# Kernel optimization log

Hardware: AMD Instinct MI355X
Metric: run time of the kernel (lower is better)

Reference implementation:

```python
import jax, jax.numpy as jnp
import numpy as np
import math

B, T, C, H = 2, 2048, 1024, 16
HD = C // H

def setup_inputs() -> dict:
    key = jax.random.key(0)
    ks = jax.random.split(key, 5)
    s_in = 1.0 / math.sqrt(C)
    x = jax.random.normal(ks[0], (B, T, C), dtype=jnp.float32)
    W_attn = jax.random.normal(ks[1], (C, 3 * C), dtype=jnp.float32) * s_in
    b_attn = jnp.zeros((3 * C,), dtype=jnp.float32)
    W_proj = jax.random.normal(ks[2], (C, C), dtype=jnp.float32) * s_in
    b_proj = jnp.zeros((C,), dtype=jnp.float32)
    return {"x": x, "W_attn": W_attn, "b_attn": b_attn, "W_proj": W_proj, "b_proj": b_proj}

def reference(x, W_attn, b_attn, W_proj, b_proj):
    Bx, Tx, Cx = x.shape
    c = x @ W_attn + b_attn  # [B,T,3C]
    q, k, v = jnp.split(c, 3, axis=2)
    # [B,T,H,hd] -> [B,H,T,hd]
    q = q.reshape(Bx, Tx, H, HD).transpose(0, 2, 1, 3)
    k = k.reshape(Bx, Tx, H, HD).transpose(0, 2, 1, 3)
    v = v.reshape(Bx, Tx, H, HD).transpose(0, 2, 1, 3)
    # NOTE: module scales by 1/sqrt(C), not 1/sqrt(head_dim)
    attn = jnp.einsum('bhqd,bhkd->bhqk', q, k) * (1.0 / math.sqrt(Cx))
    causal = jnp.tril(jnp.ones((Tx, Tx), dtype=bool))
    attn = jnp.where(causal[None, None], attn, -jnp.inf)
    attn = jax.nn.softmax(attn, axis=-1)
    y = jnp.einsum('bhqk,bhkd->bhqd', attn, v)
    y = y.transpose(0, 2, 1, 3).reshape(Bx, Tx, Cx)
    return y @ W_proj + b_proj
```

## Files before the change

### kernel.cpp

```cpp
#include <hip/hip_runtime.h>
#include <math.h>

#define Bv 2
#define Tv 2048
#define Cv 1024
#define Hv 16
#define HDv 64
#define Mv (Bv * Tv)
#define SZv (Bv * Hv * Tv * HDv)

typedef short bf16x8 __attribute__((ext_vector_type(8)));
typedef float f32x4 __attribute__((ext_vector_type(4)));

static __device__ __forceinline__ unsigned short f2bf(float f) {
    unsigned u = __float_as_uint(f);
    u += 0x7fffu + ((u >> 16) & 1u);
    return (unsigned short)(u >> 16);
}

static __device__ __forceinline__ unsigned f2bf2(float a, float b) {
    unsigned r;
    asm("v_cvt_pk_bf16_f32 %0, %1, %2" : "=v"(r) : "v"(a), "v"(b));
    return r;
}

#define AS1 __attribute__((address_space(1)))
#define AS3 __attribute__((address_space(3)))
#define GLD16(gp, lp) __builtin_amdgcn_global_load_lds( \
    (AS1 const void*)(const void*)(gp), (AS3 void*)(void*)(lp), 16, 0, 0)

#define WAITVM(n) asm volatile("s_waitcnt vmcnt(" #n ")" ::: "memory")
#define WAITLGKM0 asm volatile("s_waitcnt lgkmcnt(0)" ::: "memory")
#define BARRIER   asm volatile("s_barrier" ::: "memory")

__global__ __launch_bounds__(256) void prep_kernel(
    const float* __restrict__ x, const float* __restrict__ Wa,
    const float* __restrict__ Wp,
    unsigned short* __restrict__ xB, unsigned short* __restrict__ WaT,
    unsigned short* __restrict__ WpT)
{
    __shared__ float tile[32][33];
    const int bid = blockIdx.x;
    const int tid = threadIdx.x;

    if (bid < 4096) {
        int i = bid * 256 + tid;
        float4 f = ((const float4*)x)[i];
        ushort4 u;
        u.x = f2bf(f.x); u.y = f2bf(f.y); u.z = f2bf(f.z); u.w = f2bf(f.w);
        ((ushort4*)xB)[i] = u;
        return;
    }
    const float* src; unsigned short* dst; int Ncols, bi;
    if (bid < 7168) { bi = bid - 4096; Ncols = 3072; src = Wa; dst = WaT; }
    else            { bi = bid - 7168; Ncols = 1024; src = Wp; dst = WpT; }
    const int nct = Ncols / 32;
    const int c0 = (bi % nct) * 32, r0 = (bi / nct) * 32;
    const int tx = tid & 31, ty = tid >> 5;
    #pragma unroll
    for (int i = 0; i < 4; ++i)
        tile[ty + i * 8][tx] = src[(size_t)(r0 + ty + i * 8) * Ncols + c0 + tx];
    __syncthreads();
    #pragma unroll
    for (int i = 0; i < 4; ++i)
        dst[(size_t)(c0 + ty + i * 8) * Cv + r0 + tx] = f2bf(tile[tx][ty + i * 8]);
}

__device__ __forceinline__ void mm_mainloop_1024(
    const unsigned short* __restrict__ A, const unsigned short* __restrict__ Bt,
    unsigned short* lds, int rowBase, int colBase, f32x4 acc[4][4])
{
    const int tid  = threadIdx.x;
    const int lane = tid & 63;
    const int w    = tid >> 6;
    const int quad = lane >> 4, l15 = lane & 15;
    const int wm = (w >> 1) * 64, wn = (w & 1) * 64;
    const int K = 1024;

    const int g0 = (w * 2 + 0) * 64 + lane;
    const int g1 = (w * 2 + 1) * 64 + lane;
    const int r0 = g0 >> 2, r1 = g1 >> 2;
    const int kc0 = (g0 & 3) ^ ((r0 >> 1) & 3);
    const int kc1 = (g1 & 3) ^ ((r1 >> 1) & 3);
    const size_t offA0 = (size_t)(rowBase + r0) * K + kc0 * 8;
    const size_t offA1 = (size_t)(rowBase + r1) * K + kc1 * 8;
    const size_t offB0 = (size_t)(colBase + r0) * K + kc0 * 8;
    const size_t offB1 = (size_t)(colBase + r1) * K + kc1 * 8;
    unsigned short* ldsA0 = lds + (w * 2 + 0) * 512;
    unsigned short* ldsA1 = lds + (w * 2 + 1) * 512;
    unsigned short* ldsB0 = lds + 4096 + (w * 2 + 0) * 512;
    unsigned short* ldsB1 = lds + 4096 + (w * 2 + 1) * 512;

    const int sw = quad ^ ((l15 >> 1) & 3);
    int aoff[4], boff[4];
    #pragma unroll
    for (int i = 0; i < 4; ++i) {
        aoff[i] = ((wm + i * 16 + l15) * 4 + sw) * 8;
        boff[i] = 4096 + ((wn + i * 16 + l15) * 4 + sw) * 8;
    }

    GLD16(A + offA0, ldsA0);
    GLD16(A + offA1, ldsA1);
    GLD16(Bt + offB0, ldsB0);
    GLD16(Bt + offB1, ldsB1);
    GLD16(A + offA0 + 32, ldsA0 + 8192);
    GLD16(A + offA1 + 32, ldsA1 + 8192);
    GLD16(Bt + offB0 + 32, ldsB0 + 8192);
    GLD16(Bt + offB1 + 32, ldsB1 + 8192);

    int cur = 0;
    for (int i = 0; i < 32; ++i) {
        if (i < 31) { WAITVM(4); } else { WAITVM(0); }
        BARRIER;
        if (i < 30) {
            int nb = cur + 16384; if (nb >= 24576) nb -= 24576;
            const int k2 = (i + 2) * 32;
            GLD16(A + offA0 + k2, ldsA0 + nb);
            GLD16(A + offA1 + k2, ldsA1 + nb);
            GLD16(Bt + offB0 + k2, ldsB0 + nb);
            GLD16(Bt + offB1 + k2, ldsB1 + nb);
        }

        bf16x8 a[4], b[4];
        #pragma unroll
        for (int j = 0; j < 4; ++j) a[j] = *(const bf16x8*)(lds + cur + aoff[j]);
        #pragma unroll
        for (int j = 0; j < 4; ++j) b[j] = *(const bf16x8*)(lds + cur + boff[j]);

        #pragma unroll
        for (int mi = 0; mi < 4; ++mi)
            #pragma unroll
            for (int ni = 0; ni < 4; ++ni)
                acc[mi][ni] = __builtin_amdgcn_mfma_f32_16x16x32_bf16(
                    a[mi], b[ni], acc[mi][ni], 0, 0, 0);

        cur += 8192; if (cur == 24576) cur = 0;
    }
}

__global__ __launch_bounds__(256) void qkv_mm_kernel(
    const unsigned short* __restrict__ xB, const unsigned short* __restrict__ WaT,
    const float* __restrict__ bias,
    unsigned short* __restrict__ qB, unsigned short* __restrict__ kB,
    unsigned short* __restrict__ vT)
{
    __shared__ __align__(16) unsigned short lds[24576];
    const int rowBase = blockIdx.y * 128;
    const int colBase = blockIdx.x * 128;

    f32x4 acc[4][4];
    #pragma unroll
    for (int i = 0; i < 4; ++i)
        #pragma unroll
        for (int j = 0; j < 4; ++j) acc[i][j] = (f32x4){0.f, 0.f, 0.f, 0.f};

    mm_mainloop_1024(xB, WaT, lds, rowBase, colBase, acc);
    __syncthreads();

    const int tid = threadIdx.x, lane = tid & 63, w = tid >> 6;
    const int quad = lane >> 4, l15 = lane & 15;
    const int wm = (w >> 1) * 64, wn = (w & 1) * 64;
    const int s = colBase / Cv;
    const int tloc = rowBase & (Tv - 1);
    const int bh0 = (rowBase / Tv) * Hv + (colBase % Cv) / HDv;

    if (s < 2) {
        const float qs = (s == 0) ? 0.04508422f : 1.0f;
        #pragma unroll
        for (int mi = 0; mi < 4; ++mi)
            #pragma unroll
            for (int ni = 0; ni < 4; ++ni) {
                float bv = bias[colBase + wn + ni * 16 + l15];
                #pragma unroll
                for (int r = 0; r < 4; ++r) {
                    int m = wm + mi * 16 + quad * 4 + r;
                    int n = wn + ni * 16 + l15;
                    lds[m * 136 + n] = f2bf((acc[mi][ni][r] + bv) * qs);
                }
            }
        __syncthreads();
        unsigned short* dst = (s == 0) ? qB : kB;
        #pragma unroll
        for (int it = 0; it < 8; ++it) {
            int cc = tid + it * 256;
            int m = cc >> 4, j = cc & 15;
            uint4 v = *(const uint4*)(lds + m * 136 + j * 8);
            int hh = j >> 3, d0 = (j & 7) * 8;
            *(uint4*)(dst + ((size_t)(bh0 + hh) * Tv + tloc + m) * HDv + d0) = v;
        }
    } else {
        #pragma unroll
        for (int mi = 0; mi < 4; ++mi)
            #pragma unroll
            for (int ni = 0; ni < 4; ++ni) {
                float bv = bias[colBase + wn + ni * 16 + l15];
                #pragma unroll
                for (int r = 0; r < 4; ++r) {
                    int m = wm + mi * 16 + quad * 4 + r;
                    int n = wn + ni * 16 + l15;
                    lds[n * 136 + m] = f2bf(acc[mi][ni][r] + bv);
                }
            }
        __syncthreads();
        #pragma unroll
        for (int it = 0; it < 8; ++it) {
            int cc = tid + it * 256;
            int n = cc >> 4, j = cc & 15;
            uint4 v = *(const uint4*)(lds + n * 136 + j * 8);
            int hh = n >> 6, d = n & 63;
            *(uint4*)(vT + ((size_t)(bh0 + hh) * HDv + d) * Tv + tloc + j * 8) = v;
        }
    }
}

__global__ __launch_bounds__(256) void proj_mm_kernel(
    const unsigned short* __restrict__ y0B, const unsigned short* __restrict__ WpT,
    const float* __restrict__ bias, float* __restrict__ out)
{
    __shared__ __align__(16) unsigned short lds[24576];
    const int rowBase = blockIdx.y * 128;
    const int colBase = blockIdx.x * 128;

    f32x4 acc[4][4];
    #pragma unroll
    for (int i = 0; i < 4; ++i)
        #pragma unroll
        for (int j = 0; j < 4; ++j) acc[i][j] = (f32x4){0.f, 0.f, 0.f, 0.f};

    mm_mainloop_1024(y0B, WpT, lds, rowBase, colBase, acc);

    const int tid = threadIdx.x, lane = tid & 63, w = tid >> 6;
    const int quad = lane >> 4, l15 = lane & 15;
    const int wm = (w >> 1) * 64, wn = (w & 1) * 64;

    #pragma unroll
    for (int mi = 0; mi < 4; ++mi)
        #pragma unroll
        for (int ni = 0; ni < 4; ++ni) {
            int n = colBase + wn + ni * 16 + l15;
            float bv = bias[n];
            #pragma unroll
            for (int r = 0; r < 4; ++r) {
                int m = rowBase + wm + mi * 16 + quad * 4 + r;
                out[(size_t)m * Cv + n] = acc[mi][ni][r] + bv;
            }
        }
}

__global__ __launch_bounds__(256, 3) void attn_kernel(
    const unsigned short* __restrict__ qB, const unsigned short* __restrict__ kB,
    const unsigned short* __restrict__ vT, unsigned short* __restrict__ y0B)
{
    __shared__ __align__(16) unsigned short kv[2 * 8192];
    __shared__ __align__(16) unsigned short Pb[2][4][16 * 72];

    const int tid  = threadIdx.x;
    const int lane = tid & 63;
    const int w    = tid >> 6;
    const int quad = lane >> 4;
    const int l15  = lane & 15;

    const int qt = 31 - (blockIdx.x >> 5);
    const int bh = blockIdx.x & 31;
    const int qwbase = qt * 64 + w * 16;

    const unsigned short* qrow = qB + ((size_t)bh * Tv + qwbase + l15) * HDv;
    const bf16x8 Qa0 = *(const bf16x8*)(qrow + quad * 8);
    const bf16x8 Qa1 = *(const bf16x8*)(qrow + 32 + quad * 8);
    WAITVM(0);

    f32x4 O[4];
    float l[4] = {0.f, 0.f, 0.f, 0.f};
    #pragma unroll
    for (int n = 0; n < 4; ++n) O[n] = (f32x4){0.f, 0.f, 0.f, 0.f};

    const unsigned short* Kbase = kB + (size_t)bh * Tv * HDv;
    const unsigned short* Vbase = vT + (size_t)bh * HDv * Tv;
    unsigned short* Pw0 = &Pb[0][w][0];
    unsigned short* Pw1 = &Pb[1][w][0];

    const unsigned short* gK[2]; unsigned short* dK[2];
    const unsigned short* gV[2]; unsigned short* dV[2];
    #pragma unroll
    for (int i = 0; i < 2; ++i) {
        int slot = tid + i * 256;
        int row = slot >> 3;
        int gk = (slot & 7) ^ ((row >> 2) & 7);
        gK[i] = Kbase + row * HDv + gk * 8;
        dK[i] = kv + (size_t)(i * 256 + w * 64) * 8;
        int d = slot >> 3;
        int gv = (slot & 7) ^ (d & 7);
        gV[i] = Vbase + (size_t)d * Tv + gv * 8;
        dV[i] = kv + 4096 + (size_t)(i * 256 + w * 64) * 8;
    }

    int koff[4][2], voff[4][2];
    #pragma unroll
    for (int ct = 0; ct < 4; ++ct) {
        int row = ct + 4 * l15;
        #pragma unroll
        for (int j = 0; j < 2; ++j)
            koff[ct][j] = (row * 8 + ((quad + 4 * j) ^ (l15 & 7))) * 8;
    }
    #pragma unroll
    for (int nt = 0; nt < 4; ++nt) {
        int d = nt * 16 + l15;
        #pragma unroll
        for (int j = 0; j < 2; ++j)
            voff[nt][j] = 4096 + (d * 8 + ((quad + 4 * j) ^ (l15 & 7))) * 8;
    }

    GLD16(gK[0], dK[0]);
    GLD16(gK[1], dK[1]);
    GLD16(gV[0], dV[0]);
    GLD16(gV[1], dV[1]);

    bf16x8 Vprev[4][2];
    int cur = 0;
    for (int kt = 0; kt <= qt; ++kt) {
        WAITVM(0);
        BARRIER;
        if (kt < qt) {
            const int kb1 = (kt + 1) * 64;
            const int nxt = 8192 - cur;
            GLD16(gK[0] + (size_t)kb1 * HDv, dK[0] + nxt);
            GLD16(gK[1] + (size_t)kb1 * HDv, dK[1] + nxt);
            GLD16(gV[0] + kb1, dV[0] + nxt);
            GLD16(gV[1] + kb1, dV[1] + nxt);
        }

        unsigned short* PwW = (kt & 1) ? Pw1 : Pw0;
        unsigned short* PwR = (kt & 1) ? Pw0 : Pw1;

        if (kt > 0) {
            const bf16x8 Pa0 = *(const bf16x8*)(PwR + l15 * 72 + quad * 8);
            const bf16x8 Pa1 = *(const bf16x8*)(PwR + l15 * 72 + 32 + quad * 8);
            #pragma unroll
            for (int nt = 0; nt < 4; ++nt) {
                O[nt] = __builtin_amdgcn_mfma_f32_16x16x32_bf16(Pa0, Vprev[nt][0], O[nt], 0, 0, 0);
                O[nt] = __builtin_amdgcn_mfma_f32_16x16x32_bf16(Pa1, Vprev[nt][1], O[nt], 0, 0, 0);
            }
        }

        bf16x8 Kb[4][2];
        #pragma unroll
        for (int ct = 0; ct < 4; ++ct) {
            Kb[ct][0] = *(const bf16x8*)(kv + cur + koff[ct][0]);
            Kb[ct][1] = *(const bf16x8*)(kv + cur + koff[ct][1]);
        }
        f32x4 S[4];
        #pragma unroll
        for (int ct = 0; ct < 4; ++ct) {
            S[ct] = (f32x4){0.f, 0.f, 0.f, 0.f};
            S[ct] = __builtin_amdgcn_mfma_f32_16x16x32_bf16(Qa0, Kb[ct][0], S[ct], 0, 0, 0);
            S[ct] = __builtin_amdgcn_mfma_f32_16x16x32_bf16(Qa1, Kb[ct][1], S[ct], 0, 0, 0);
        }

        #pragma unroll
        for (int nt = 0; nt < 4; ++nt) {
            Vprev[nt][0] = *(const bf16x8*)(kv + cur + voff[nt][0]);
            Vprev[nt][1] = *(const bf16x8*)(kv + cur + voff[nt][1]);
        }

        if (kt == qt) {
            #pragma unroll
            for (int ct = 0; ct < 4; ++ct)
                #pragma unroll
                for (int r = 0; r < 4; ++r)
                    if (ct + 4 * l15 > w * 16 + quad * 4 + r) S[ct][r] = -1e30f;
        }

        float p[4][4];
        #pragma unroll
        for (int ct = 0; ct < 4; ++ct)
            #pragma unroll
            for (int r = 0; r < 4; ++r)
                p[ct][r] = __builtin_amdgcn_exp2f(S[ct][r]);
        #pragma unroll
        for (int r = 0; r < 4; ++r)
            l[r] += (p[0][r] + p[1][r]) + (p[2][r] + p[3][r]);

        #pragma unroll
        for (int r = 0; r < 4; ++r) {
            uint2 u = make_uint2(f2bf2(p[0][r], p[1][r]), f2bf2(p[2][r], p[3][r]));
            *(uint2*)(PwW + (quad * 4 + r) * 72 + l15 * 4) = u;
        }

        cur = 8192 - cur;
    }

    {
        unsigned short* PwR = (qt & 1) ? Pw1 : Pw0;
        const bf16x8 Pa0 = *(const bf16x8*)(PwR + l15 * 72 + quad * 8);
        const bf16x8 Pa1 = *(const bf16x8*)(PwR + l15 * 72 + 32 + quad * 8);
        #pragma unroll
        for (int nt = 0; nt < 4; ++nt) {
            O[nt] = __builtin_amdgcn_mfma_f32_16x16x32_bf16(Pa0, Vprev[nt][0], O[nt], 0, 0, 0);
            O[nt] = __builtin_amdgcn_mfma_f32_16x16x32_bf16(Pa1, Vprev[nt][1], O[nt], 0, 0, 0);
        }
    }

    #pragma unroll
    for (int r = 0; r < 4; ++r) {
        l[r] += __shfl_xor(l[r], 1);
        l[r] += __shfl_xor(l[r], 2);
        l[r] += __shfl_xor(l[r], 4);
        l[r] += __shfl_xor(l[r], 8);
    }

    const int b = bh >> 4, h = bh & 15;
    #pragma unroll
    for (int r = 0; r < 4; ++r) {
        float inv = 1.f / l[r];
        int q = qwbase + quad * 4 + r;
        unsigned short* dst = y0B + ((size_t)(b * Tv + q)) * Cv + h * HDv + l15;
        #pragma unroll
        for (int n = 0; n < 4; ++n) dst[n * 16] = f2bf(O[n][r] * inv);
    }
}

extern "C" void kernel_launch(void* const* d_in, const int* in_sizes, int n_in,
                              void* d_out, int out_size, void* d_ws, size_t ws_size,
                              hipStream_t stream) {
    const float* x      = (const float*)d_in[0];
    const float* W_attn = (const float*)d_in[1];
    const float* b_attn = (const float*)d_in[2];
    const float* W_proj = (const float*)d_in[3];
    const float* b_proj = (const float*)d_in[4];
    float* out = (float*)d_out;

    unsigned short* xB  = (unsigned short*)d_ws;
    unsigned short* WaT = xB  + (size_t)Mv * Cv;
    unsigned short* WpT = WaT + (size_t)3 * Cv * Cv;
    unsigned short* qB  = WpT + (size_t)Cv * Cv;
    unsigned short* kB  = qB + (size_t)SZv;
    unsigned short* vT  = kB + (size_t)SZv;
    unsigned short* y0B = vT + (size_t)SZv;

    dim3 blk(256);
    prep_kernel<<<dim3(8192), blk, 0, stream>>>(x, W_attn, W_proj, xB, WaT, WpT);
    qkv_mm_kernel<<<dim3(3 * Cv / 128, Mv / 128), blk, 0, stream>>>(xB, WaT, b_attn, qB, kB, vT);
    attn_kernel<<<dim3(Bv * Hv * (Tv / 64)), blk, 0, stream>>>(qB, kB, vT, y0B);
    proj_mm_kernel<<<dim3(Cv / 128, Mv / 128), blk, 0, stream>>>(y0B, WpT, b_proj, out);
}
```

Baseline: 163.6 us.

## Load GEMM operands directly from global into registers, dropping LDS staging

Result: slower. 234.7 us (+43.4%).

```diff
diff --git a/kernel.cpp b/kernel.cpp
--- a/kernel.cpp
+++ b/kernel.cpp
@@ -68,83 +68,56 @@
 
 __device__ __forceinline__ void mm_mainloop_1024(
     const unsigned short* __restrict__ A, const unsigned short* __restrict__ Bt,
-    unsigned short* lds, int rowBase, int colBase, f32x4 acc[4][4])
+    int rowBase, int colBase, f32x4 acc[4][4])
 {
-    const int tid  = threadIdx.x;
-    const int lane = tid & 63;
-    const int w    = tid >> 6;
+    const int lane = threadIdx.x & 63;
+    const int w    = threadIdx.x >> 6;
     const int quad = lane >> 4, l15 = lane & 15;
     const int wm = (w >> 1) * 64, wn = (w & 1) * 64;
     const int K = 1024;
 
-    const int g0 = (w * 2 + 0) * 64 + lane;
-    const int g1 = (w * 2 + 1) * 64 + lane;
-    const int r0 = g0 >> 2, r1 = g1 >> 2;
-    const int kc0 = (g0 & 3) ^ ((r0 >> 1) & 3);
-    const int kc1 = (g1 & 3) ^ ((r1 >> 1) & 3);
-    const size_t offA0 = (size_t)(rowBase + r0) * K + kc0 * 8;
-    const size_t offA1 = (size_t)(rowBase + r1) * K + kc1 * 8;
-    const size_t offB0 = (size_t)(colBase + r0) * K + kc0 * 8;
-    const size_t offB1 = (size_t)(colBase + r1) * K + kc1 * 8;
-    unsigned short* ldsA0 = lds + (w * 2 + 0) * 512;
-    unsigned short* ldsA1 = lds + (w * 2 + 1) * 512;
-    unsigned short* ldsB0 = lds + 4096 + (w * 2 + 0) * 512;
-    unsigned short* ldsB1 = lds + 4096 + (w * 2 + 1) * 512;
-
-    const int sw = quad ^ ((l15 >> 1) & 3);
-    int aoff[4], boff[4];
+    const unsigned short* ap[4];
+    const unsigned short* bp[4];
     #pragma unroll
     for (int i = 0; i < 4; ++i) {
-        aoff[i] = ((wm + i * 16 + l15) * 4 + sw) * 8;
-        boff[i] = 4096 + ((wn + i * 16 + l15) * 4 + sw) * 8;
-    }
-
-    GLD16(A + offA0, ldsA0);
-    GLD16(A + offA1, ldsA1);
-    GLD16(Bt + offB0, ldsB0);
-    GLD16(Bt + offB1, ldsB1);
-    GLD16(A + offA0 + 32, ldsA0 + 8192);
-    GLD16(A + offA1 + 32, ldsA1 + 8192);
-    GLD16(Bt + offB0 + 32, ldsB0 + 8192);
-    GLD16(Bt + offB1 + 32, ldsB1 + 8192);
-
-    int cur = 0;
+        ap[i] = A  + (size_t)(rowBase + wm + i * 16 + l15) * K + quad * 8;
+        bp[i] = Bt + (size_t)(colBase + wn + i * 16 + l15) * K + quad * 8;
+    }
+
+    bf16x8 a[2][4], b[2][4];
+    #pragma unroll
+    for (int j = 0; j < 4; ++j) {
+        a[0][j] = *(const bf16x8*)(ap[j]);
+        b[0][j] = *(const bf16x8*)(bp[j]);
+    }
+
+    #pragma unroll 2
     for (int i = 0; i < 32; ++i) {
-        if (i < 31) { WAITVM(4); } else { WAITVM(0); }
-        BARRIER;
-        if (i < 30) {
-            int nb = cur + 16384; if (nb >= 24576) nb -= 24576;
-            const int k2 = (i + 2) * 32;
-            GLD16(A + offA0 + k2, ldsA0 + nb);
-            GLD16(A + offA1 + k2, ldsA1 + nb);
-            GLD16(Bt + offB0 + k2, ldsB0 + nb);
-            GLD16(Bt + offB1 + k2, ldsB1 + nb);
-        }
-
-        bf16x8 a[4], b[4];
-        #pragma unroll
-        for (int j = 0; j < 4; ++j) a[j] = *(const bf16x8*)(lds + cur + aoff[j]);
-        #pragma unroll
-        for (int j = 0; j < 4; ++j) b[j] = *(const bf16x8*)(lds + cur + boff[j]);
-
+        const int cur = i & 1, nxt = cur ^ 1;
+        if (i < 31) {
+            const int k1 = (i + 1) * 32;
+            #pragma unroll
+            for (int j = 0; j < 4; ++j) {
+                a[nxt][j] = *(const bf16x8*)(ap[j] + k1);
+                b[nxt][j] = *(const bf16x8*)(bp[j] + k1);
+            }
+        }
         #pragma unroll
         for (int mi = 0; mi < 4; ++mi)
             #pragma unroll
             for (int ni = 0; ni < 4; ++ni)
                 acc[mi][ni] = __builtin_amdgcn_mfma_f32_16x16x32_bf16(
-                    a[mi], b[ni], acc[mi][ni], 0, 0, 0);
-
-        cur += 8192; if (cur == 24576) cur = 0;
-    }
-}
-
-__global__ __launch_bounds__(256) void qkv_mm_kernel(
+                    a[cur][mi], b[cur][ni], acc[mi][ni], 0, 0, 0);
+    }
+}
+
+__global__ __launch_bounds__(256, 2) void qkv_mm_kernel(
     const unsigned short* __restrict__ xB, const unsigned short* __restrict__ WaT,
     const float* __restrict__ bias,
     unsigned short* __restrict__ qB, unsigned short* __restrict__ kB,
     unsigned short* __restrict__ vT)
 {
-    __shared__ __align__(16) unsigned short lds[24576];
+    __shared__ __align__(16) unsigned short lds[128 * 136];
     const int rowBase = blockIdx.y * 128;
     const int colBase = blockIdx.x * 128;
 
@@ -154,8 +127,7 @@
         #pragma unroll
         for (int j = 0; j < 4; ++j) acc[i][j] = (f32x4){0.f, 0.f, 0.f, 0.f};
 
-    mm_mainloop_1024(xB, WaT, lds, rowBase, colBase, acc);
-    __syncthreads();
+    mm_mainloop_1024(xB, WaT, rowBase, colBase, acc);
 
     const int tid = threadIdx.x, lane = tid & 63, w = tid >> 6;
     const int quad = lane >> 4, l15 = lane & 15;
@@ -213,11 +185,10 @@
     }
 }
 
-__global__ __launch_bounds__(256) void proj_mm_kernel(
+__global__ __launch_bounds__(256, 2) void proj_mm_kernel(
     const unsigned short* __restrict__ y0B, const unsigned short* __restrict__ WpT,
     const float* __restrict__ bias, float* __restrict__ out)
 {
-    __shared__ __align__(16) unsigned short lds[24576];
     const int rowBase = blockIdx.y * 128;
     const int colBase = blockIdx.x * 128;
 
@@ -227,7 +198,7 @@
         #pragma unroll
         for (int j = 0; j < 4; ++j) acc[i][j] = (f32x4){0.f, 0.f, 0.f, 0.f};
 
-    mm_mainloop_1024(y0B, WpT, lds, rowBase, colBase, acc);
+    mm_mainloop_1024(y0B, WpT, rowBase, colBase, acc);
 
     const int tid = threadIdx.x, lane = tid & 63, w = tid >> 6;
     const int quad = lane >> 4, l15 = lane & 15;
```

## Use 64x128 tiles with a three-stage LDS pipeline in the projection GEMM

Applied to the files above, without the earlier changes.

Result: no change. 164.8 us (+0.7%).

```diff
diff --git a/kernel.cpp b/kernel.cpp
--- a/kernel.cpp
+++ b/kernel.cpp
@@ -217,24 +217,80 @@
     const unsigned short* __restrict__ y0B, const unsigned short* __restrict__ WpT,
     const float* __restrict__ bias, float* __restrict__ out)
 {
-    __shared__ __align__(16) unsigned short lds[24576];
-    const int rowBase = blockIdx.y * 128;
+    __shared__ __align__(16) unsigned short lds[18432];
+    const int rowBase = blockIdx.y * 64;
     const int colBase = blockIdx.x * 128;
-
-    f32x4 acc[4][4];
-    #pragma unroll
-    for (int i = 0; i < 4; ++i)
+    const int K = 1024;
+
+    const int tid  = threadIdx.x;
+    const int lane = tid & 63;
+    const int w    = tid >> 6;
+    const int quad = lane >> 4, l15 = lane & 15;
+    const int wm = (w >> 1) * 32, wn = (w & 1) * 64;
+
+    const int gA = tid;
+    const int rA = gA >> 2, kcA = (gA & 3) ^ ((rA >> 1) & 3);
+    const unsigned short* gpA = y0B + (size_t)(rowBase + rA) * K + kcA * 8;
+    unsigned short* ldA = lds + (size_t)(w * 64) * 8;
+
+    const int gB0 = tid, gB1 = 256 + tid;
+    const int rB0 = gB0 >> 2, kcB0 = (gB0 & 3) ^ ((rB0 >> 1) & 3);
+    const int rB1 = gB1 >> 2, kcB1 = (gB1 & 3) ^ ((rB1 >> 1) & 3);
+    const unsigned short* gpB0 = WpT + (size_t)(colBase + rB0) * K + kcB0 * 8;
+    const unsigned short* gpB1 = WpT + (size_t)(colBase + rB1) * K + kcB1 * 8;
+    unsigned short* ldB0 = lds + 2048 + (size_t)(w * 64) * 8;
+    unsigned short* ldB1 = lds + 2048 + (size_t)(256 + w * 64) * 8;
+
+    const int sw = quad ^ ((l15 >> 1) & 3);
+    int aoff[2], boff[4];
+    #pragma unroll
+    for (int i = 0; i < 2; ++i) aoff[i] = ((wm + i * 16 + l15) * 4 + sw) * 8;
+    #pragma unroll
+    for (int i = 0; i < 4; ++i) boff[i] = 2048 + ((wn + i * 16 + l15) * 4 + sw) * 8;
+
+    f32x4 acc[2][4];
+    #pragma unroll
+    for (int i = 0; i < 2; ++i)
         #pragma unroll
         for (int j = 0; j < 4; ++j) acc[i][j] = (f32x4){0.f, 0.f, 0.f, 0.f};
 
-    mm_mainloop_1024(y0B, WpT, lds, rowBase, colBase, acc);
-
-    const int tid = threadIdx.x, lane = tid & 63, w = tid >> 6;
-    const int quad = lane >> 4, l15 = lane & 15;
-    const int wm = (w >> 1) * 64, wn = (w & 1) * 64;
-
-    #pragma unroll
-    for (int mi = 0; mi < 4; ++mi)
+    GLD16(gpA, ldA);
+    GLD16(gpB0, ldB0);
+    GLD16(gpB1, ldB1);
+    GLD16(gpA + 32, ldA + 6144);
+    GLD16(gpB0 + 32, ldB0 + 6144);
+    GLD16(gpB1 + 32, ldB1 + 6144);
+
+    int cur = 0;
+    for (int i = 0; i < 32; ++i) {
+        if (i < 31) { WAITVM(3); } else { WAITVM(0); }
+        BARRIER;
+        if (i < 30) {
+            int nb = cur + 12288; if (nb >= 18432) nb -= 18432;
+            const int k2 = (i + 2) * 32;
+            GLD16(gpA + k2, ldA + nb);
+            GLD16(gpB0 + k2, ldB0 + nb);
+            GLD16(gpB1 + k2, ldB1 + nb);
+        }
+
+        bf16x8 a[2], b[4];
+        #pragma unroll
+        for (int j = 0; j < 2; ++j) a[j] = *(const bf16x8*)(lds + cur + aoff[j]);
+        #pragma unroll
+        for (int j = 0; j < 4; ++j) b[j] = *(const bf16x8*)(lds + cur + boff[j]);
+
+        #pragma unroll
+        for (int mi = 0; mi < 2; ++mi)
+            #pragma unroll
+            for (int ni = 0; ni < 4; ++ni)
+                acc[mi][ni] = __builtin_amdgcn_mfma_f32_16x16x32_bf16(
+                    a[mi], b[ni], acc[mi][ni], 0, 0, 0);
+
+        cur += 6144; if (cur == 18432) cur = 0;
+    }
+
+    #pragma unroll
+    for (int mi = 0; mi < 2; ++mi)
         #pragma unroll
         for (int ni = 0; ni < 4; ++ni) {
             int n = colBase + wn + ni * 16 + l15;
@@ -441,5 +497,5 @@
     prep_kernel<<<dim3(8192), blk, 0, stream>>>(x, W_attn, W_proj, xB, WaT, WpT);
     qkv_mm_kernel<<<dim3(3 * Cv / 128, Mv / 128), blk, 0, stream>>>(xB, WaT, b_attn, qB, kB, vT);
     attn_kernel<<<dim3(Bv * Hv * (Tv / 64)), blk, 0, stream>>>(qB, kB, vT, y0B);
-    proj_mm_kernel<<<dim3(Cv / 128, Mv / 128), blk, 0, stream>>>(y0B, WpT, b_proj, out);
-}
+    proj_mm_kernel<<<dim3(Cv / 128, Mv / 64), blk, 0, stream>>>(y0B, WpT, b_proj, out);
+}
```
